# Kernel optimization log

Measured on AMD Instinct MI355X. Metric: run time of the kernel, lower is better.

## Reference

```python
import jax, jax.numpy as jnp
import numpy as np

T, B, OBS, H, A = 512, 64, 512, 1024, 18


def setup_inputs() -> dict:
    key = jax.random.key(0)
    ks = jax.random.split(key, 8)
    s = lambda fan: 1.0 / np.sqrt(fan)
    return {
        "obs": jax.random.normal(ks[0], (T, B, OBS), jnp.float32),
        # binary done/valid mask per (timestep, env)
        "mask": (jax.random.uniform(ks[1], (T, B)) > 0.05).astype(jnp.float32),
        "W_enc": jax.random.normal(ks[2], (H, OBS), jnp.float32) * s(OBS),
        "b_enc": jnp.zeros((H,), jnp.float32),
        "W_ih": jax.random.normal(ks[3], (4 * H, H), jnp.float32) * s(H),
        "b_ih": jnp.zeros((4 * H,), jnp.float32),
        "W_hh": jax.random.normal(ks[4], (4 * H, H), jnp.float32) * s(H),
        "b_hh": jnp.zeros((4 * H,), jnp.float32),
        "W_dec": jax.random.normal(ks[5], (A, H), jnp.float32) * s(H),
        "b_dec": jnp.zeros((A,), jnp.float32),
    }


def reference(obs, mask, W_enc, b_enc, W_ih, b_ih, W_hh, b_hh, W_dec, b_dec):
    # encoder MLP + relu, batched over all T*B (one big GEMM)
    encoded = jax.nn.relu(jnp.einsum("tbo,ho->tbh", obs, W_enc) + b_enc)
    # precompute input contribution to LSTM gates for all timesteps: [T,B,4H]
    x_gates = jnp.einsum("tbh,gh->tbg", encoded, W_ih) + b_ih + b_hh

    def step(carry, inp):
        h, c = carry
        xg, m = inp  # xg: [B,4H], m: [B]
        gates = xg + h @ W_hh.T
        i, f, g, o = jnp.split(gates, 4, axis=-1)  # torch LSTMCell order
        c_new = jax.nn.sigmoid(f) * c + jax.nn.sigmoid(i) * jnp.tanh(g)
        h_new = jax.nn.sigmoid(o) * jnp.tanh(c_new)
        m = m[:, None]
        h_new = h_new * m
        c_new = c_new * m
        return (h_new, c_new), h_new

    h0 = jnp.zeros((B, H), jnp.float32)
    c0 = jnp.zeros((B, H), jnp.float32)
    (h, c), latent = jax.lax.scan(step, (h0, c0), (x_gates, mask))

    # decoder over flattened (T*B, H) then mask q-values
    values = jnp.einsum("tbh,ah->tba", latent, W_dec) + b_dec
    values = values * mask[..., None]
    return values, h, c
```

## Files before the change

### kernel.cpp

```cpp
#include <hip/hip_runtime.h>
#include <hip/hip_bf16.h>

#define T_ 512
#define B_ 64
#define OBS_ 512
#define H_ 1024
#define A_ 18
#define MM_ (T_*B_)
#define G4_ (4*H_)
#define CH_ 64
#define NCH_ (T_/CH_)
#define CM_ (CH_*B_)

typedef unsigned short u16;
typedef unsigned long long u64;
typedef __attribute__((ext_vector_type(8))) short s8v;
typedef __attribute__((ext_vector_type(4))) float f4v;

__device__ __forceinline__ float b2f(u16 u){
    unsigned x = ((unsigned)u) << 16;
    return __builtin_bit_cast(float, x);
}
__device__ __forceinline__ u16 f2b(float f){
    unsigned x = __builtin_bit_cast(unsigned, f);
    return (u16)((x + 0x7fffu + ((x >> 16) & 1u)) >> 16);
}

__device__ __forceinline__ float fsig(float x){
    return __builtin_amdgcn_rcpf(1.f + __expf(-x));
}
__device__ __forceinline__ float ftanh(float x){
    return 1.f - 2.f * __builtin_amdgcn_rcpf(__expf(2.f * x) + 1.f);
}


__global__ void prep_all(const float* __restrict__ Wenc, const float* __restrict__ Wih,
                         const float* __restrict__ Whh, const float* __restrict__ Wdec,
                         const float* __restrict__ bih, const float* __restrict__ bhh,
                         u16* __restrict__ wenc_b, u16* __restrict__ wih_b,
                         u16* __restrict__ whh_b, u16* __restrict__ wdec_b,
                         float* __restrict__ bias2, u16* __restrict__ h_hist,
                         float* __restrict__ c_f32, unsigned* __restrict__ flags)
{
    int i = blockIdx.x * blockDim.x + threadIdx.x;
    int stride = gridDim.x * blockDim.x;
    for (int k = i; k < G4_ * H_; k += stride){
        wih_b[k] = f2b(Wih[k]);
        whh_b[k] = f2b(Whh[k]);
    }
    for (int k = i; k < H_ * OBS_; k += stride) wenc_b[k] = f2b(Wenc[k]);
    for (int k = i; k < A_ * H_; k += stride) wdec_b[k] = f2b(Wdec[k]);
    for (int k = i; k < G4_; k += stride) bias2[k] = bih[k] + bhh[k];
    unsigned* h0 = (unsigned*)h_hist;
    for (int k = i; k < B_ * H_ / 2; k += stride) h0[k] = 0u;
    for (int k = i; k < B_ * H_; k += stride) c_f32[k] = 0.f;
    for (int k = i; k < 1024; k += stride) flags[k] = 0u;
}

__global__ void copy_hc(const float* __restrict__ h, const float* __restrict__ c,
                        float* __restrict__ out){
    int i = blockIdx.x * blockDim.x + threadIdx.x;
    out[(size_t)MM_*A_ + i] = h[i];
    out[(size_t)MM_*A_ + B_*H_ + i] = c[i];
}


#define LDSS 72

template<bool A_FP32, bool RELU>
__global__ __launch_bounds__(256) void gemm_bt(
    const void* __restrict__ Aptr, const u16* __restrict__ W,
    const float* __restrict__ bias, u16* __restrict__ C,
    int M, int N, int K)
{
    __shared__ __align__(16) u16 As[128 * LDSS];
    __shared__ __align__(16) u16 Bs[128 * LDSS];

    const int tid  = threadIdx.x;
    const int lane = tid & 63;
    const int wid  = tid >> 6;
    const int wm   = wid & 1, wn = wid >> 1;
    const int m0   = blockIdx.y * 128, n0 = blockIdx.x * 128;
    const int quad = lane >> 4, l16 = lane & 15;

    f4v acc[4][4];
    #pragma unroll
    for (int i = 0; i < 4; i++)
        #pragma unroll
        for (int j = 0; j < 4; j++) acc[i][j] = (f4v){0.f,0.f,0.f,0.f};

    for (int k0 = 0; k0 < K; k0 += 64){
        __syncthreads();
        if (A_FP32){
            const float* A = (const float*)Aptr;
            #pragma unroll
            for (int pss = 0; pss < 8; pss++){
                int idx = pss * 256 + tid;
                int row = idx >> 4, ch = idx & 15;
                float4 v = *(const float4*)(A + (size_t)(m0 + row) * K + k0 + ch * 4);
                u16* d = &As[row * LDSS + ch * 4];
                d[0] = f2b(v.x); d[1] = f2b(v.y); d[2] = f2b(v.z); d[3] = f2b(v.w);
            }
        } else {
            const u16* A = (const u16*)Aptr;
            #pragma unroll
            for (int pss = 0; pss < 4; pss++){
                int idx = pss * 256 + tid;
                int row = idx >> 3, ch = idx & 7;
                *(uint4*)&As[row * LDSS + ch * 8] =
                    *(const uint4*)(A + (size_t)(m0 + row) * K + k0 + ch * 8);
            }
        }
        #pragma unroll
        for (int pss = 0; pss < 4; pss++){
            int idx = pss * 256 + tid;
            int row = idx >> 3, ch = idx & 7;
            *(uint4*)&Bs[row * LDSS + ch * 8] =
                *(const uint4*)(W + (size_t)(n0 + row) * K + k0 + ch * 8);
        }
        __syncthreads();

        #pragma unroll
        for (int kk = 0; kk < 64; kk += 32){
            s8v af[4], bf[4];
            #pragma unroll
            for (int mt = 0; mt < 4; mt++)
                af[mt] = *(const s8v*)&As[(wm*64 + mt*16 + l16) * LDSS + kk + quad*8];
            #pragma unroll
            for (int nt = 0; nt < 4; nt++)
                bf[nt] = *(const s8v*)&Bs[(wn*64 + nt*16 + l16) * LDSS + kk + quad*8];
            #pragma unroll
            for (int mt = 0; mt < 4; mt++)
                #pragma unroll
                for (int nt = 0; nt < 4; nt++)
                    acc[mt][nt] = __builtin_amdgcn_mfma_f32_16x16x32_bf16(
                        af[mt], bf[nt], acc[mt][nt], 0, 0, 0);
        }
    }

    #pragma unroll
    for (int mt = 0; mt < 4; mt++){
        #pragma unroll
        for (int nt = 0; nt < 4; nt++){
            #pragma unroll
            for (int r = 0; r < 4; r++){
                int m = m0 + wm*64 + mt*16 + quad*4 + r;
                int n = n0 + wn*64 + nt*16 + l16;
                float v = acc[mt][nt][r] + bias[n];
                if (RELU) v = fmaxf(v, 0.f);
                C[(size_t)m * N + n] = f2b(v);
            }
        }
    }
}


__global__ __launch_bounds__(256, 1) void lstm_scan(
    const u16* __restrict__ xg,
    const u16* __restrict__ Whh,
    u16* __restrict__ h_hist,
    float* __restrict__ c_glob,
    float* __restrict__ h_f32,
    const float* __restrict__ mask,
    unsigned* __restrict__ flags,
    int t0)
{
    __shared__ float red[4][4][16][17];

    const int tid  = threadIdx.x;
    const int lane = tid & 63;
    const int w    = tid >> 6;
    const int quad = lane >> 4, l16 = lane & 15;
    const int bid  = blockIdx.x;
    const int g = bid & 3, s = bid >> 2;
    const int rb0 = g * 16, j0 = s * 16;

    const int koff = w * 256;
    s8v bf[4][8];
    #pragma unroll
    for (int gate = 0; gate < 4; gate++)
        #pragma unroll
        for (int ks = 0; ks < 8; ks++)
            bf[gate][ks] = *(const s8v*)(
                Whh + (size_t)(gate * H_ + j0 + l16) * H_ + koff + ks * 32 + quad * 8);

    const int cb = tid >> 4, cu = tid & 15;
    const size_t cidx = (size_t)(rb0 + cb) * H_ + j0 + cu;
    float c_reg = c_glob[cidx];

    const size_t hoff = (size_t)(rb0 + l16) * H_ + koff + quad * 8;

    unsigned* myflag = flags + (g << 8) + (s << 2) + w;
    const unsigned* pollp = flags + (g << 8) + (w << 6) + lane;

    const u16* xg0 = xg + (size_t)(rb0 + cb) * G4_ + j0 + cu;
    u16 nxi = xg0[0], nxf = xg0[H_], nxv = xg0[2 * H_], nxo = xg0[3 * H_];
    float nm = mask[rb0 + cb];

    for (int st = 0; st < CH_; st++){
        const float xi = b2f(nxi), xf = b2f(nxf), xv = b2f(nxv), xo = b2f(nxo);
        const float m = nm;

        const unsigned tgt = (unsigned)(t0 + st);
        int tries = 0;
        for (;;){
            unsigned f = __hip_atomic_load(pollp, __ATOMIC_RELAXED, __HIP_MEMORY_SCOPE_AGENT);
            if (__all((int)(f >= tgt))) break;
            if (++tries > (1 << 20)) break;
            if (tries >= 8) __builtin_amdgcn_s_sleep(1);
        }

        const u16* hs = h_hist + (size_t)st * B_ * H_ + hoff;
        f4v acc[4];
        #pragma unroll
        for (int gate = 0; gate < 4; gate++) acc[gate] = (f4v){0.f,0.f,0.f,0.f};
        #pragma unroll
        for (int ks = 0; ks < 8; ks++){
            s8v af = *(const s8v*)(hs + ks * 32);
            #pragma unroll
            for (int gate = 0; gate < 4; gate++)
                acc[gate] = __builtin_amdgcn_mfma_f32_16x16x32_bf16(af, bf[gate][ks], acc[gate], 0, 0, 0);
        }
        #pragma unroll
        for (int gate = 0; gate < 4; gate++)
            #pragma unroll
            for (int r = 0; r < 4; r++)
                red[w][gate][quad * 4 + r][l16] = acc[gate][r];
        __syncthreads();

        float gi = xi, gf = xf, gg = xv, go = xo;
        #pragma unroll
        for (int ww = 0; ww < 4; ww++){
            gi += red[ww][0][cb][cu];
            gf += red[ww][1][cb][cu];
            gg += red[ww][2][cb][cu];
            go += red[ww][3][cb][cu];
        }

        float is = fsig(gi);
        float fs = fsig(gf);
        float os = fsig(go);
        float gt = ftanh(gg);

        float cn = fs * c_reg + is * gt;
        float hn = os * ftanh(cn);
        hn *= m; cn *= m;
        c_reg = cn;
        if (t0 + st == T_ - 1) h_f32[cidx] = hn;

        unsigned hb = (unsigned)f2b(hn);
        unsigned partner = (unsigned)__shfl_xor((int)hb, 1, 64);
        if ((cu & 1) == 0){
            unsigned packed = hb | (partner << 16);
            unsigned* dst = (unsigned*)(h_hist + (size_t)(st + 1) * B_ * H_ + cidx);
            __hip_atomic_store(dst, packed, __ATOMIC_RELAXED, __HIP_MEMORY_SCOPE_AGENT);
            if (st == CH_ - 1){
                unsigned* dst0 = (unsigned*)(h_hist + cidx);
                __hip_atomic_store(dst0, packed, __ATOMIC_RELAXED, __HIP_MEMORY_SCOPE_AGENT);
            }
        }
        asm volatile("s_waitcnt vmcnt(0)" ::: "memory");

        if (lane == 0)
            __hip_atomic_store(myflag, (unsigned)(t0 + st + 1),
                               __ATOMIC_RELAXED, __HIP_MEMORY_SCOPE_AGENT);

        if (st + 1 < CH_){
            const u16* xgn = xg + (size_t)(st + 1) * B_ * G4_ + (size_t)(rb0 + cb) * G4_ + j0 + cu;
            nxi = xgn[0]; nxf = xgn[H_]; nxv = xgn[2 * H_]; nxo = xgn[3 * H_];
            nm = mask[(size_t)(st + 1) * B_ + rb0 + cb];
        }

        __syncthreads();
    }

    c_glob[cidx] = c_reg;
}


__global__ __launch_bounds__(256) void decode_kernel(
    const u16* __restrict__ latent, const u16* __restrict__ Wdec,
    const float* __restrict__ bdec, const float* __restrict__ mask,
    float* __restrict__ values, int rows)
{
    __shared__ __align__(16) u16 wl[A_ * H_];
    const int tid = threadIdx.x;
    for (int i = tid; i < A_ * H_ / 8; i += 256)
        ((uint4*)wl)[i] = ((const uint4*)Wdec)[i];
    __syncthreads();

    const int lane = tid & 63;
    int wid = blockIdx.x * 4 + (tid >> 6);
    const int nwaves = gridDim.x * 4;

    for (int row = wid; row < rows; row += nwaves){
        float lat[16];
        #pragma unroll
        for (int i = 0; i < 16; i++)
            lat[i] = b2f(latent[(size_t)row * H_ + i*64 + lane]);
        float acc[A_];
        #pragma unroll
        for (int a = 0; a < A_; a++) acc[a] = 0.f;
        #pragma unroll
        for (int i = 0; i < 16; i++){
            #pragma unroll
            for (int a = 0; a < A_; a++)
                acc[a] += lat[i] * b2f(wl[a * H_ + i*64 + lane]);
        }
        float m = mask[row];
        #pragma unroll
        for (int a = 0; a < A_; a++){
            float v = acc[a];
            #pragma unroll
            for (int s = 32; s > 0; s >>= 1) v += __shfl_down(v, s, 64);
            if (lane == 0) values[(size_t)row * A_ + a] = (v + bdec[a]) * m;
        }
    }
}


extern "C" void kernel_launch(void* const* d_in, const int* in_sizes, int n_in,
                              void* d_out, int out_size, void* d_ws, size_t ws_size,
                              hipStream_t stream)
{
    const float* obs  = (const float*)d_in[0];
    const float* mask = (const float*)d_in[1];
    const float* Wenc = (const float*)d_in[2];
    const float* benc = (const float*)d_in[3];
    const float* Wih  = (const float*)d_in[4];
    const float* bih  = (const float*)d_in[5];
    const float* Whh  = (const float*)d_in[6];
    const float* bhh  = (const float*)d_in[7];
    const float* Wdec = (const float*)d_in[8];
    const float* bdec = (const float*)d_in[9];
    float* out = (float*)d_out;

    char* p = (char*)d_ws;
    size_t o = 0;
    auto alloc = [&](size_t bytes){ void* r = p + o; o += (bytes + 255) & ~(size_t)255; return r; };
    u16*      wenc_b  = (u16*)     alloc((size_t)H_ * OBS_ * 2);
    u16*      wih_b   = (u16*)     alloc((size_t)G4_ * H_ * 2);
    u16*      whh_b   = (u16*)     alloc((size_t)G4_ * H_ * 2);
    u16*      wdec_b  = (u16*)     alloc((size_t)A_ * H_ * 2);
    float*    bias2   = (float*)   alloc((size_t)G4_ * 4);
    u16*      h_hist  = (u16*)     alloc((size_t)(CH_ + 1) * B_ * H_ * 2);
    float*    h_f32   = (float*)   alloc((size_t)B_ * H_ * 4);
    float*    c_f32   = (float*)   alloc((size_t)B_ * H_ * 4);
    unsigned* flags   = (unsigned*)alloc(1024 * 4);
    u16*      xg_ch   = (u16*)     alloc((size_t)CM_ * G4_ * 2);

    const size_t enc_all_b = (size_t)MM_ * H_ * 2;
    const bool big = ws_size >= o + enc_all_b + 4096;
    (void)in_sizes; (void)n_in; (void)out_size;

    prep_all<<<2048, 256, 0, stream>>>(Wenc, Wih, Whh, Wdec, bih, bhh,
                                       wenc_b, wih_b, whh_b, wdec_b,
                                       bias2, h_hist, c_f32, flags);

    if (big){
        u16* enc_all = (u16*)alloc(enc_all_b);

        dim3 ge(H_ / 128, MM_ / 128);
        gemm_bt<true, true><<<ge, 256, 0, stream>>>(
            obs, wenc_b, benc, enc_all, MM_, H_, OBS_);

        for (int c = 0; c < NCH_; c++){
            const int t0 = c * CH_;

            dim3 gx(G4_ / 128, CM_ / 128);
            gemm_bt<false, false><<<gx, 256, 0, stream>>>(
                enc_all + (size_t)c * CM_ * H_, wih_b, bias2, xg_ch, CM_, G4_, H_);

            lstm_scan<<<256, 256, 0, stream>>>(
                xg_ch, whh_b, h_hist, c_f32, h_f32,
                mask + (size_t)t0 * B_, flags, t0);

            decode_kernel<<<256, 256, 0, stream>>>(
                h_hist + (size_t)B_ * H_, wdec_b, bdec, mask + (size_t)t0 * B_,
                out + (size_t)t0 * B_ * A_, CM_);
        }
    } else {
        u16* enc_ch = (u16*)alloc((size_t)CM_ * H_ * 2);

        for (int c = 0; c < NCH_; c++){
            const int t0 = c * CH_;

            dim3 g1(H_ / 128, CM_ / 128);
            gemm_bt<true, true><<<g1, 256, 0, stream>>>(
                obs + (size_t)t0 * B_ * OBS_, wenc_b, benc, enc_ch, CM_, H_, OBS_);

            dim3 g2(G4_ / 128, CM_ / 128);
            gemm_bt<false, false><<<g2, 256, 0, stream>>>(
                enc_ch, wih_b, bias2, xg_ch, CM_, G4_, H_);

            lstm_scan<<<256, 256, 0, stream>>>(
                xg_ch, whh_b, h_hist, c_f32, h_f32,
                mask + (size_t)t0 * B_, flags, t0);

            decode_kernel<<<256, 256, 0, stream>>>(
                h_hist + (size_t)B_ * H_, wdec_b, bdec, mask + (size_t)t0 * B_,
                out + (size_t)t0 * B_ * A_, CM_);
        }
    }

    copy_hc<<<256, 256, 0, stream>>>(h_f32, c_f32, out);
}
```

Baseline: 2.575 ms.

## Run whole-sequence GEMMs once, single persistent LSTM scan, async global-to-LDS loads

On the large-workspace path, the input-gate GEMM now runs once over all timesteps instead of per chunk. A single persistent lstm_scan launch then covers all 512 steps, and one decode launch follows. This removes the per-chunk launch chain and the grid re-sync and weight reload that each new scan launch paid. It also pre-converts obs to bf16 in the prep kernel, switches GEMM tile loads to global_load_lds with an unpadded LDS layout, and prefetches the next flag value inside the poll loop. In exchange it needs much more workspace (full h history and full xg), and the unpadded LDS rows may cause bank conflicts on the fragment reads.

```diff
diff --git a/kernel.cpp b/kernel.cpp
--- a/kernel.cpp
+++ b/kernel.cpp
@@ -33,13 +33,21 @@
     return 1.f - 2.f * __builtin_amdgcn_rcpf(__expf(2.f * x) + 1.f);
 }
 
+__device__ __forceinline__ void gl_lds16(const u16* g, u16* l){
+    __builtin_amdgcn_global_load_lds(
+        (const __attribute__((address_space(1))) unsigned int*)g,
+        (__attribute__((address_space(3))) unsigned int*)l, 16, 0, 0);
+}
+
 
 __global__ void prep_all(const float* __restrict__ Wenc, const float* __restrict__ Wih,
                          const float* __restrict__ Whh, const float* __restrict__ Wdec,
                          const float* __restrict__ bih, const float* __restrict__ bhh,
+                         const float* __restrict__ obs,
                          u16* __restrict__ wenc_b, u16* __restrict__ wih_b,
                          u16* __restrict__ whh_b, u16* __restrict__ wdec_b,
-                         float* __restrict__ bias2, u16* __restrict__ h_hist,
+                         float* __restrict__ bias2, u16* __restrict__ obs_b,
+                         u16* __restrict__ h0buf,
                          float* __restrict__ c_f32, unsigned* __restrict__ flags)
 {
     int i = blockIdx.x * blockDim.x + threadIdx.x;
@@ -48,10 +56,11 @@
         wih_b[k] = f2b(Wih[k]);
         whh_b[k] = f2b(Whh[k]);
     }
+    for (int k = i; k < MM_ * OBS_; k += stride) obs_b[k] = f2b(obs[k]);
     for (int k = i; k < H_ * OBS_; k += stride) wenc_b[k] = f2b(Wenc[k]);
     for (int k = i; k < A_ * H_; k += stride) wdec_b[k] = f2b(Wdec[k]);
     for (int k = i; k < G4_; k += stride) bias2[k] = bih[k] + bhh[k];
-    unsigned* h0 = (unsigned*)h_hist;
+    unsigned* h0 = (unsigned*)h0buf;
     for (int k = i; k < B_ * H_ / 2; k += stride) h0[k] = 0u;
     for (int k = i; k < B_ * H_; k += stride) c_f32[k] = 0.f;
     for (int k = i; k < 1024; k += stride) flags[k] = 0u;
@@ -65,16 +74,14 @@
 }
 
 
-#define LDSS 72
-
-template<bool A_FP32, bool RELU>
+template<bool RELU>
 __global__ __launch_bounds__(256) void gemm_bt(
-    const void* __restrict__ Aptr, const u16* __restrict__ W,
+    const u16* __restrict__ A, const u16* __restrict__ W,
     const float* __restrict__ bias, u16* __restrict__ C,
     int M, int N, int K)
 {
-    __shared__ __align__(16) u16 As[128 * LDSS];
-    __shared__ __align__(16) u16 Bs[128 * LDSS];
+    __shared__ __align__(16) u16 As[128 * 64];
+    __shared__ __align__(16) u16 Bs[128 * 64];
 
     const int tid  = threadIdx.x;
     const int lane = tid & 63;
@@ -91,33 +98,14 @@
 
     for (int k0 = 0; k0 < K; k0 += 64){
         __syncthreads();
-        if (A_FP32){
-            const float* A = (const float*)Aptr;
-            #pragma unroll
-            for (int pss = 0; pss < 8; pss++){
-                int idx = pss * 256 + tid;
-                int row = idx >> 4, ch = idx & 15;
-                float4 v = *(const float4*)(A + (size_t)(m0 + row) * K + k0 + ch * 4);
-                u16* d = &As[row * LDSS + ch * 4];
-                d[0] = f2b(v.x); d[1] = f2b(v.y); d[2] = f2b(v.z); d[3] = f2b(v.w);
-            }
-        } else {
-            const u16* A = (const u16*)Aptr;
-            #pragma unroll
-            for (int pss = 0; pss < 4; pss++){
-                int idx = pss * 256 + tid;
-                int row = idx >> 3, ch = idx & 7;
-                *(uint4*)&As[row * LDSS + ch * 8] =
-                    *(const uint4*)(A + (size_t)(m0 + row) * K + k0 + ch * 8);
-            }
-        }
-        #pragma unroll
-        for (int pss = 0; pss < 4; pss++){
-            int idx = pss * 256 + tid;
+        #pragma unroll
+        for (int ps = 0; ps < 4; ps++){
+            int idx = ps * 256 + tid;
             int row = idx >> 3, ch = idx & 7;
-            *(uint4*)&Bs[row * LDSS + ch * 8] =
-                *(const uint4*)(W + (size_t)(n0 + row) * K + k0 + ch * 8);
-        }
+            gl_lds16(A + (size_t)(m0 + row) * K + k0 + ch * 8, &As[idx * 8]);
+            gl_lds16(W + (size_t)(n0 + row) * K + k0 + ch * 8, &Bs[idx * 8]);
+        }
+        asm volatile("s_waitcnt vmcnt(0)" ::: "memory");
         __syncthreads();
 
         #pragma unroll
@@ -125,10 +113,10 @@
             s8v af[4], bf[4];
             #pragma unroll
             for (int mt = 0; mt < 4; mt++)
-                af[mt] = *(const s8v*)&As[(wm*64 + mt*16 + l16) * LDSS + kk + quad*8];
+                af[mt] = *(const s8v*)&As[(wm*64 + mt*16 + l16) * 64 + kk + quad*8];
             #pragma unroll
             for (int nt = 0; nt < 4; nt++)
-                bf[nt] = *(const s8v*)&Bs[(wn*64 + nt*16 + l16) * LDSS + kk + quad*8];
+                bf[nt] = *(const s8v*)&Bs[(wn*64 + nt*16 + l16) * 64 + kk + quad*8];
             #pragma unroll
             for (int mt = 0; mt < 4; mt++)
                 #pragma unroll
@@ -163,7 +151,7 @@
     float* __restrict__ h_f32,
     const float* __restrict__ mask,
     unsigned* __restrict__ flags,
-    int t0)
+    int t0, int nsteps, u16* __restrict__ seed)
 {
     __shared__ float red[4][4][16][17];
 
@@ -197,17 +185,21 @@
     u16 nxi = xg0[0], nxf = xg0[H_], nxv = xg0[2 * H_], nxo = xg0[3 * H_];
     float nm = mask[rb0 + cb];
 
-    for (int st = 0; st < CH_; st++){
+    for (int st = 0; st < nsteps; st++){
         const float xi = b2f(nxi), xf = b2f(nxf), xv = b2f(nxv), xo = b2f(nxo);
         const float m = nm;
 
         const unsigned tgt = (unsigned)(t0 + st);
-        int tries = 0;
-        for (;;){
+        {
             unsigned f = __hip_atomic_load(pollp, __ATOMIC_RELAXED, __HIP_MEMORY_SCOPE_AGENT);
-            if (__all((int)(f >= tgt))) break;
-            if (++tries > (1 << 20)) break;
-            if (tries >= 8) __builtin_amdgcn_s_sleep(1);
+            int tries = 0;
+            for (;;){
+                unsigned fn = __hip_atomic_load(pollp, __ATOMIC_RELAXED, __HIP_MEMORY_SCOPE_AGENT);
+                if (__all((int)(f >= tgt))) break;
+                f = fn;
+                if (++tries > (1 << 20)) break;
+                if (tries >= 8) __builtin_amdgcn_s_sleep(1);
+            }
         }
 
         const u16* hs = h_hist + (size_t)st * B_ * H_ + hoff;
@@ -254,8 +246,8 @@
             unsigned packed = hb | (partner << 16);
             unsigned* dst = (unsigned*)(h_hist + (size_t)(st + 1) * B_ * H_ + cidx);
             __hip_atomic_store(dst, packed, __ATOMIC_RELAXED, __HIP_MEMORY_SCOPE_AGENT);
-            if (st == CH_ - 1){
-                unsigned* dst0 = (unsigned*)(h_hist + cidx);
+            if (seed && st == nsteps - 1){
+                unsigned* dst0 = (unsigned*)(seed + cidx);
                 __hip_atomic_store(dst0, packed, __ATOMIC_RELAXED, __HIP_MEMORY_SCOPE_AGENT);
             }
         }
@@ -265,7 +257,7 @@
             __hip_atomic_store(myflag, (unsigned)(t0 + st + 1),
                                __ATOMIC_RELAXED, __HIP_MEMORY_SCOPE_AGENT);
 
-        if (st + 1 < CH_){
+        if (st + 1 < nsteps){
             const u16* xgn = xg + (size_t)(st + 1) * B_ * G4_ + (size_t)(rb0 + cb) * G4_ + j0 + cu;
             nxi = xgn[0]; nxf = xgn[H_]; nxv = xgn[2 * H_]; nxo = xgn[3 * H_];
             nm = mask[(size_t)(st + 1) * B_ + rb0 + cb];
@@ -343,64 +335,67 @@
     u16*      whh_b   = (u16*)     alloc((size_t)G4_ * H_ * 2);
     u16*      wdec_b  = (u16*)     alloc((size_t)A_ * H_ * 2);
     float*    bias2   = (float*)   alloc((size_t)G4_ * 4);
-    u16*      h_hist  = (u16*)     alloc((size_t)(CH_ + 1) * B_ * H_ * 2);
+    u16*      obs_b   = (u16*)     alloc((size_t)MM_ * OBS_ * 2);
     float*    h_f32   = (float*)   alloc((size_t)B_ * H_ * 4);
     float*    c_f32   = (float*)   alloc((size_t)B_ * H_ * 4);
     unsigned* flags   = (unsigned*)alloc(1024 * 4);
-    u16*      xg_ch   = (u16*)     alloc((size_t)CM_ * G4_ * 2);
-
+
+    const size_t hall_b    = (size_t)(T_ + 1) * B_ * H_ * 2;
     const size_t enc_all_b = (size_t)MM_ * H_ * 2;
-    const bool big = ws_size >= o + enc_all_b + 4096;
+    const size_t xg_all_b  = (size_t)MM_ * G4_ * 2;
+    const bool big = ws_size >= o + hall_b + enc_all_b + xg_all_b + 65536;
     (void)in_sizes; (void)n_in; (void)out_size;
 
-    prep_all<<<2048, 256, 0, stream>>>(Wenc, Wih, Whh, Wdec, bih, bhh,
-                                       wenc_b, wih_b, whh_b, wdec_b,
-                                       bias2, h_hist, c_f32, flags);
-
     if (big){
+        u16* h_all   = (u16*)alloc(hall_b);
         u16* enc_all = (u16*)alloc(enc_all_b);
+        u16* xg_all  = (u16*)alloc(xg_all_b);
+
+        prep_all<<<2048, 256, 0, stream>>>(Wenc, Wih, Whh, Wdec, bih, bhh, obs,
+                                           wenc_b, wih_b, whh_b, wdec_b,
+                                           bias2, obs_b, h_all, c_f32, flags);
 
         dim3 ge(H_ / 128, MM_ / 128);
-        gemm_bt<true, true><<<ge, 256, 0, stream>>>(
-            obs, wenc_b, benc, enc_all, MM_, H_, OBS_);
+        gemm_bt<true><<<ge, 256, 0, stream>>>(
+            obs_b, wenc_b, benc, enc_all, MM_, H_, OBS_);
+
+        dim3 gx(G4_ / 128, MM_ / 128);
+        gemm_bt<false><<<gx, 256, 0, stream>>>(
+            enc_all, wih_b, bias2, xg_all, MM_, G4_, H_);
+
+        lstm_scan<<<256, 256, 0, stream>>>(
+            xg_all, whh_b, h_all, c_f32, h_f32, mask, flags, 0, T_, nullptr);
+
+        decode_kernel<<<2048, 256, 0, stream>>>(
+            h_all + (size_t)B_ * H_, wdec_b, bdec, mask, out, MM_);
+    } else {
+        u16* h_hist = (u16*)alloc((size_t)(CH_ + 1) * B_ * H_ * 2);
+        u16* enc_ch = (u16*)alloc((size_t)CM_ * H_ * 2);
+        u16* xg_ch  = (u16*)alloc((size_t)CM_ * G4_ * 2);
+
+        prep_all<<<2048, 256, 0, stream>>>(Wenc, Wih, Whh, Wdec, bih, bhh, obs,
+                                           wenc_b, wih_b, whh_b, wdec_b,
+                                           bias2, obs_b, h_hist, c_f32, flags);
 
         for (int c = 0; c < NCH_; c++){
             const int t0 = c * CH_;
 
-            dim3 gx(G4_ / 128, CM_ / 128);
-            gemm_bt<false, false><<<gx, 256, 0, stream>>>(
-                enc_all + (size_t)c * CM_ * H_, wih_b, bias2, xg_ch, CM_, G4_, H_);
+            dim3 g1(H_ / 128, CM_ / 128);
+            gemm_bt<true><<<g1, 256, 0, stream>>>(
+                obs_b + (size_t)t0 * B_ * OBS_, wenc_b, benc, enc_ch, CM_, H_, OBS_);
+
+            dim3 g2(G4_ / 128, CM_ / 128);
+            gemm_bt<false><<<g2, 256, 0, stream>>>(
+                enc_ch, wih_b, bias2, xg_ch, CM_, G4_, H_);
 
             lstm_scan<<<256, 256, 0, stream>>>(
                 xg_ch, whh_b, h_hist, c_f32, h_f32,
-                mask + (size_t)t0 * B_, flags, t0);
+                mask + (size_t)t0 * B_, flags, t0, CH_, h_hist);
 
             decode_kernel<<<256, 256, 0, stream>>>(
                 h_hist + (size_t)B_ * H_, wdec_b, bdec, mask + (size_t)t0 * B_,
                 out + (size_t)t0 * B_ * A_, CM_);
         }
-    } else {
-        u16* enc_ch = (u16*)alloc((size_t)CM_ * H_ * 2);
-
-        for (int c = 0; c < NCH_; c++){
-            const int t0 = c * CH_;
-
-            dim3 g1(H_ / 128, CM_ / 128);
-            gemm_bt<true, true><<<g1, 256, 0, stream>>>(
-                obs + (size_t)t0 * B_ * OBS_, wenc_b, benc, enc_ch, CM_, H_, OBS_);
-
-            dim3 g2(G4_ / 128, CM_ / 128);
-            gemm_bt<false, false><<<g2, 256, 0, stream>>>(
-                enc_ch, wih_b, bias2, xg_ch, CM_, G4_, H_);
-
-            lstm_scan<<<256, 256, 0, stream>>>(
-                xg_ch, whh_b, h_hist, c_f32, h_f32,
-                mask + (size_t)t0 * B_, flags, t0);
-
-            decode_kernel<<<256, 256, 0, stream>>>(
-                h_hist + (size_t)B_ * H_, wdec_b, bdec, mask + (size_t)t0 * B_,
-                out + (size_t)t0 * B_ * A_, CM_);
-        }
     }
 
     copy_hc<<<256, 256, 0, stream>>>(h_f32, c_f32, out);
```

Result: slower. 2.652 ms (+3.0%).
